# Optimization experiments

Hardware: AMD Instinct MI355X
Metric: run time of the kernel (lower is better)

Reference implementation:

```python
import jax, jax.numpy as jnp
import numpy as np

D_MODEL = 1024
N_HEADS = 16
HEAD_DIM = D_MODEL // N_HEADS


def setup_inputs() -> dict:
    key = jax.random.key(0)
    ks = jax.random.split(key, 5)
    x = jax.random.normal(ks[0], (2, 2048, D_MODEL), dtype=jnp.float32)
    s = 1.0 / np.sqrt(D_MODEL)
    W_qkv = jax.random.normal(ks[1], (D_MODEL, 3 * D_MODEL), dtype=jnp.float32) * s
    b_qkv = jnp.zeros((3 * D_MODEL,), dtype=jnp.float32)
    W_proj = jax.random.normal(ks[2], (D_MODEL, D_MODEL), dtype=jnp.float32) * s
    b_proj = jnp.zeros((D_MODEL,), dtype=jnp.float32)
    return {"x": x, "W_qkv": W_qkv, "b_qkv": b_qkv, "W_proj": W_proj, "b_proj": b_proj}


def reference(x, W_qkv, b_qkv, W_proj, b_proj):
    b, t, c = x.shape
    qkv = x @ W_qkv + b_qkv  # [b,t,3c]
    q, k, v = jnp.split(qkv, 3, axis=-1)
    # [b, h, t, d]
    q = q.reshape(b, t, N_HEADS, HEAD_DIM).transpose(0, 2, 1, 3)
    k = k.reshape(b, t, N_HEADS, HEAD_DIM).transpose(0, 2, 1, 3)
    v = v.reshape(b, t, N_HEADS, HEAD_DIM).transpose(0, 2, 1, 3)
    att = jnp.einsum('bhqd,bhkd->bhqk', q, k) / np.sqrt(HEAD_DIM)
    causal = jnp.tril(jnp.ones((t, t), dtype=bool))  # [t,t]
    att = jnp.where(causal[None, None], att, -jnp.inf)
    att = jax.nn.softmax(att, axis=-1)
    out = jnp.einsum('bhqk,bhkd->bhqd', att, v)  # [b,h,t,d]
    out = out.transpose(0, 2, 1, 3).reshape(b, t, c)
    return out @ W_proj + b_proj
```

## Files before the change

kernel.cpp:

```cpp
#include <hip/hip_runtime.h>
#include <hip/hip_bf16.h>

#define NB 2
#define NH 16
#define HD 64
#define DM 1024
#define TT 2048

typedef __attribute__((ext_vector_type(4))) float f32x4;
typedef __attribute__((ext_vector_type(8))) short bf16x8;

__device__ __forceinline__ unsigned short f2bf(float f) {
  union { float f; unsigned int i; } x; x.f = f;
  unsigned int r = x.i + 0x7fffu + ((x.i >> 16) & 1u);
  return (unsigned short)(r >> 16);
}

__device__ __forceinline__ unsigned int cvtpk(float lo, float hi) {
  unsigned int r;
  asm("v_cvt_pk_bf16_f32 %0, %1, %2" : "=v"(r) : "v"(lo), "v"(hi));
  return r;
}

__device__ __forceinline__ void async16(unsigned short* lds_base, const unsigned short* g) {
  __builtin_amdgcn_global_load_lds(
      (const __attribute__((address_space(1))) void*)g,
      (__attribute__((address_space(3))) void*)lds_base, 16, 0, 0);
}

__global__ __launch_bounds__(256)
void prep_kernel(const float* __restrict__ x, unsigned short* __restrict__ xbf,
                 const float* __restrict__ Wqkv, unsigned short* __restrict__ WqkvT,
                 const float* __restrict__ Wproj, unsigned short* __restrict__ WprojT)
{
  __shared__ unsigned short T[64][72];
  const int bid = blockIdx.x;
  const int t = threadIdx.x;

  if (bid < 2048) {
    const int i = bid * 256 + t;
    const f32x4 a = *(const f32x4*)(x + (size_t)i * 8);
    const f32x4 b = *(const f32x4*)(x + (size_t)i * 8 + 4);
    uint4 o;
    o.x = f2bf(a.x) | ((unsigned)f2bf(a.y) << 16);
    o.y = f2bf(a.z) | ((unsigned)f2bf(a.w) << 16);
    o.z = f2bf(b.x) | ((unsigned)f2bf(b.y) << 16);
    o.w = f2bf(b.z) | ((unsigned)f2bf(b.w) << 16);
    *(uint4*)(xbf + (size_t)i * 8) = o;
    return;
  }

  const float* W;
  unsigned short* WT;
  int n0, k0, N;
  if (bid < 2048 + 768) {
    const int li = bid - 2048;
    W = Wqkv; WT = WqkvT; N = 3 * DM;
    n0 = (li % 48) * 64; k0 = (li / 48) * 64;
  } else {
    const int li = bid - 2816;
    W = Wproj; WT = WprojT; N = DM;
    n0 = (li % 16) * 64; k0 = (li / 16) * 64;
  }
  const int r = t >> 2;
  const int c = (t & 3) * 16;
  const float* src = W + (size_t)(k0 + r) * N + n0 + c;
  #pragma unroll
  for (int s = 0; s < 4; ++s) {
    const f32x4 v = *(const f32x4*)(src + s * 4);
    T[c + s*4 + 0][r] = f2bf(v.x);
    T[c + s*4 + 1][r] = f2bf(v.y);
    T[c + s*4 + 2][r] = f2bf(v.z);
    T[c + s*4 + 3][r] = f2bf(v.w);
  }
  __syncthreads();
  unsigned short* dst = WT + (size_t)(n0 + r) * DM + k0 + c;
  *(uint4*)(dst)     = *(const uint4*)(&T[r][c]);
  *(uint4*)(dst + 8) = *(const uint4*)(&T[r][c + 8]);
}

__global__ __launch_bounds__(256)
void gemm_qkv(const unsigned short* __restrict__ A, const unsigned short* __restrict__ BT,
              const float* __restrict__ bias, unsigned short* __restrict__ Cout,
              int M, int N, int K)
{
  __shared__ unsigned short As[128 * 32];
  __shared__ unsigned short Bs[128 * 32];
  const int tid = threadIdx.x;
  const int lane = tid & 63;
  const int w = tid >> 6;
  const int wr = w >> 1, wc = w & 1;
  const int l15 = lane & 15, g = lane >> 4;

  const int gx = gridDim.x;
  const int li = blockIdx.y * gx + blockIdx.x;
  const int chunk = (gx * gridDim.y) >> 3;
  const int tile = (li & 7) * chunk + (li >> 3);
  const int m0 = (tile / gx) * 128;
  const int n0 = (tile % gx) * 128;

  f32x4 acc[4][4] = {};

  const int ar0 = tid >> 2,          as0 = (tid & 3) * 8;
  const int ar1 = (256 + tid) >> 2;
  const unsigned short* A0 = A + (size_t)(m0 + ar0) * K + as0;
  const unsigned short* A1 = A + (size_t)(m0 + ar1) * K + as0;
  const unsigned short* B0 = BT + (size_t)(n0 + ar0) * K + as0;
  const unsigned short* B1 = BT + (size_t)(n0 + ar1) * K + as0;
  unsigned short* AsW0 = &As[(0 * 256 + w * 64) * 8];
  unsigned short* AsW1 = &As[(1 * 256 + w * 64) * 8];
  unsigned short* BsW0 = &Bs[(0 * 256 + w * 64) * 8];
  unsigned short* BsW1 = &Bs[(1 * 256 + w * 64) * 8];

  for (int k0 = 0; k0 < K; k0 += 32) {
    async16(AsW0, A0 + k0);
    async16(AsW1, A1 + k0);
    async16(BsW0, B0 + k0);
    async16(BsW1, B1 + k0);
    __syncthreads();

    bf16x8 af[4], bfv[4];
    #pragma unroll
    for (int i = 0; i < 4; ++i)
      af[i] = *(const bf16x8*)(&As[(wr * 64 + i * 16 + l15) * 32 + g * 8]);
    #pragma unroll
    for (int j = 0; j < 4; ++j)
      bfv[j] = *(const bf16x8*)(&Bs[(wc * 64 + j * 16 + l15) * 32 + g * 8]);
    #pragma unroll
    for (int i = 0; i < 4; ++i)
      #pragma unroll
      for (int j = 0; j < 4; ++j)
        acc[i][j] = __builtin_amdgcn_mfma_f32_16x16x32_bf16(af[i], bfv[j], acc[i][j], 0, 0, 0);
    __syncthreads();
  }

  #pragma unroll
  for (int i = 0; i < 4; ++i) {
    #pragma unroll
    for (int j = 0; j < 4; ++j) {
      #pragma unroll
      for (int e = 0; e < 4; ++e) {
        const int row = m0 + wr * 64 + i * 16 + g * 4 + e;
        const int col = n0 + wc * 64 + j * 16 + l15;
        float val = acc[i][j][e] + bias[col];
        const int which = col >> 10;
        if (which == 0) val *= 0.125f;
        const int rem = col & 1023;
        const int hh = rem >> 6, dd = rem & 63;
        const int bb = row >> 11, tt = row & 2047;
        Cout[((((size_t)which * NB + bb) * NH + hh) * TT + tt) * HD + dd] = f2bf(val);
      }
    }
  }
}

__global__ __launch_bounds__(256)
void gemm_proj(const unsigned short* __restrict__ A, const unsigned short* __restrict__ BT,
               const float* __restrict__ bias, float* __restrict__ Cout,
               int M, int N, int K)
{
  __shared__ unsigned short As[128 * 32];
  __shared__ unsigned short Bs[64 * 32];
  const int tid = threadIdx.x;
  const int lane = tid & 63;
  const int w = tid >> 6;
  const int wr = w >> 1, wc = w & 1;
  const int l15 = lane & 15, g = lane >> 4;

  const int gx = gridDim.x;
  const int li = blockIdx.y * gx + blockIdx.x;
  const int chunk = (gx * gridDim.y) >> 3;
  const int tile = (li & 7) * chunk + (li >> 3);
  const int m0 = (tile / gx) * 128;
  const int n0 = (tile % gx) * 64;

  f32x4 acc[4][2] = {};

  const int ar0 = tid >> 2,          as0 = (tid & 3) * 8;
  const int ar1 = (256 + tid) >> 2;
  const unsigned short* A0 = A + (size_t)(m0 + ar0) * K + as0;
  const unsigned short* A1 = A + (size_t)(m0 + ar1) * K + as0;
  const unsigned short* B0 = BT + (size_t)(n0 + ar0) * K + as0;
  unsigned short* AsW0 = &As[(0 * 256 + w * 64) * 8];
  unsigned short* AsW1 = &As[(1 * 256 + w * 64) * 8];
  unsigned short* BsW0 = &Bs[(w * 64) * 8];

  for (int k0 = 0; k0 < K; k0 += 32) {
    async16(AsW0, A0 + k0);
    async16(AsW1, A1 + k0);
    async16(BsW0, B0 + k0);
    __syncthreads();

    bf16x8 af[4], bfv[2];
    #pragma unroll
    for (int i = 0; i < 4; ++i)
      af[i] = *(const bf16x8*)(&As[(wr * 64 + i * 16 + l15) * 32 + g * 8]);
    #pragma unroll
    for (int j = 0; j < 2; ++j)
      bfv[j] = *(const bf16x8*)(&Bs[(wc * 32 + j * 16 + l15) * 32 + g * 8]);
    #pragma unroll
    for (int i = 0; i < 4; ++i)
      #pragma unroll
      for (int j = 0; j < 2; ++j)
        acc[i][j] = __builtin_amdgcn_mfma_f32_16x16x32_bf16(af[i], bfv[j], acc[i][j], 0, 0, 0);
    __syncthreads();
  }

  #pragma unroll
  for (int i = 0; i < 4; ++i) {
    #pragma unroll
    for (int j = 0; j < 2; ++j) {
      #pragma unroll
      for (int e = 0; e < 4; ++e) {
        const int row = m0 + wr * 64 + i * 16 + g * 4 + e;
        const int col = n0 + wc * 32 + j * 16 + l15;
        Cout[(size_t)row * N + col] = acc[i][j][e] + bias[col];
      }
    }
  }
}

__global__ __launch_bounds__(512)
void attn_kernel(const unsigned short* __restrict__ qkv, unsigned short* __restrict__ attn_out)
{
  __shared__ unsigned short Ksm[64 * 72];
  __shared__ unsigned short VTsm[64 * 70];
  __shared__ unsigned short Psm[8][16 * 72];

  const int tid = threadIdx.x;
  const int lane = tid & 63;
  const int wv = tid >> 6;
  const int l15 = lane & 15;
  const int g = lane >> 4;

  const int li = blockIdx.x;
  const int xcd = li & 7;
  const int r = li >> 3;
  const int halfid = r >> 5;
  const int j = r & 31;
  const int bh = ((j >> 3) << 3) | xcd;
  const int jj = j & 7;
  const int qt = halfid ? (7 - jj) : (8 + jj);
  const int q0 = qt * 128;

  const size_t base = (size_t)bh * TT * HD;
  const unsigned short* Qg = qkv + base;
  const unsigned short* Kg = qkv + (size_t)NB * NH * TT * HD + base;
  const unsigned short* Vg = qkv + (size_t)2 * NB * NH * TT * HD + base;

  const int qw = q0 + wv * 16;
  const bf16x8 qf0 = *(const bf16x8*)(Qg + (size_t)(qw + l15) * HD + g * 8);
  const bf16x8 qf1 = *(const bf16x8*)(Qg + (size_t)(qw + l15) * HD + 32 + g * 8);

  f32x4 o[4] = {};
  float lsum = 0.f;

  const bool kRole = (wv < 4);
  const int krow = (tid & 255) >> 2;
  const int kseg = (tid & 3) * 16;
  const int vt   = tid & 255;
  const int vr0  = (vt >> 4) * 4;
  const int vc0  = (vt & 15) * 4;

  const int nt = 2 * qt + 2;

  uint4 st0, st1;
  {
    if (kRole) {
      const unsigned short* kp = Kg + (size_t)krow * HD + kseg;
      st0 = *(const uint4*)(kp);
      st1 = *(const uint4*)(kp + 8);
    } else {
      const uint2 a = *(const uint2*)(Vg + (size_t)(vr0 + 0) * HD + vc0);
      const uint2 b = *(const uint2*)(Vg + (size_t)(vr0 + 1) * HD + vc0);
      const uint2 c = *(const uint2*)(Vg + (size_t)(vr0 + 2) * HD + vc0);
      const uint2 d = *(const uint2*)(Vg + (size_t)(vr0 + 3) * HD + vc0);
      st0.x = a.x; st0.y = a.y; st0.z = b.x; st0.w = b.y;
      st1.x = c.x; st1.y = c.y; st1.z = d.x; st1.w = d.y;
    }
  }

  for (int t = 0; t < nt; ++t) {
    const int t0 = t * 64;
    __syncthreads();
    if (kRole) {
      *(uint4*)(&Ksm[krow * 72 + kseg])     = st0;
      *(uint4*)(&Ksm[krow * 72 + kseg + 8]) = st1;
    } else {
      unsigned short r0[4] = {(unsigned short)(st0.x & 0xffffu), (unsigned short)(st0.x >> 16),
                              (unsigned short)(st0.y & 0xffffu), (unsigned short)(st0.y >> 16)};
      unsigned short r1[4] = {(unsigned short)(st0.z & 0xffffu), (unsigned short)(st0.z >> 16),
                              (unsigned short)(st0.w & 0xffffu), (unsigned short)(st0.w >> 16)};
      unsigned short r2[4] = {(unsigned short)(st1.x & 0xffffu), (unsigned short)(st1.x >> 16),
                              (unsigned short)(st1.y & 0xffffu), (unsigned short)(st1.y >> 16)};
      unsigned short r3[4] = {(unsigned short)(st1.z & 0xffffu), (unsigned short)(st1.z >> 16),
                              (unsigned short)(st1.w & 0xffffu), (unsigned short)(st1.w >> 16)};
      #pragma unroll
      for (int c2 = 0; c2 < 4; ++c2) {
        ushort4 col;
        col.x = r0[c2]; col.y = r1[c2]; col.z = r2[c2]; col.w = r3[c2];
        *(ushort4*)(&VTsm[(vc0 + c2) * 70 + vr0]) = col;
      }
    }
    __syncthreads();

    if (t + 1 < nt) {
      const int t1 = t0 + 64;
      if (kRole) {
        const unsigned short* kp = Kg + (size_t)(t1 + krow) * HD + kseg;
        st0 = *(const uint4*)(kp);
        st1 = *(const uint4*)(kp + 8);
      } else {
        const uint2 a = *(const uint2*)(Vg + (size_t)(t1 + vr0 + 0) * HD + vc0);
        const uint2 b = *(const uint2*)(Vg + (size_t)(t1 + vr0 + 1) * HD + vc0);
        const uint2 c = *(const uint2*)(Vg + (size_t)(t1 + vr0 + 2) * HD + vc0);
        const uint2 d = *(const uint2*)(Vg + (size_t)(t1 + vr0 + 3) * HD + vc0);
        st0.x = a.x; st0.y = a.y; st0.z = b.x; st0.w = b.y;
        st1.x = c.x; st1.y = c.y; st1.z = d.x; st1.w = d.y;
      }
    }

    if (t0 <= qw + 15) {
      f32x4 sT[4] = {};
      __builtin_amdgcn_s_setprio(1);
      #pragma unroll
      for (int b = 0; b < 4; ++b) {
        const bf16x8 kf0 = *(const bf16x8*)(&Ksm[(b * 16 + l15) * 72 + g * 8]);
        const bf16x8 kf1 = *(const bf16x8*)(&Ksm[(b * 16 + l15) * 72 + 32 + g * 8]);
        sT[b] = __builtin_amdgcn_mfma_f32_16x16x32_bf16(kf0, qf0, sT[b], 0, 0, 0);
        sT[b] = __builtin_amdgcn_mfma_f32_16x16x32_bf16(kf1, qf1, sT[b], 0, 0, 0);
      }
      __builtin_amdgcn_s_setprio(0);

      if (t0 + 63 > qw) {
        #pragma unroll
        for (int b = 0; b < 4; ++b)
          #pragma unroll
          for (int e = 0; e < 4; ++e)
            if (t0 + b * 16 + 4 * g + e > qw + l15) sT[b][e] = -INFINITY;
      }

      #pragma unroll
      for (int b = 0; b < 4; ++b) {
        const float p0 = __expf(sT[b][0]);
        const float p1 = __expf(sT[b][1]);
        const float p2 = __expf(sT[b][2]);
        const float p3 = __expf(sT[b][3]);
        lsum += (p0 + p1) + (p2 + p3);
        uint2 wd; wd.x = cvtpk(p0, p1); wd.y = cvtpk(p2, p3);
        *(uint2*)(&Psm[wv][l15 * 72 + b * 16 + 4 * g]) = wd;
      }

      __builtin_amdgcn_s_setprio(1);
      #pragma unroll
      for (int c = 0; c < 2; ++c) {
        const bf16x8 pf = *(const bf16x8*)(&Psm[wv][l15 * 72 + c * 32 + g * 8]);
        #pragma unroll
        for (int db = 0; db < 4; ++db) {
          const bf16x8 vf = *(const bf16x8*)(&VTsm[(db * 16 + l15) * 70 + c * 32 + g * 8]);
          o[db] = __builtin_amdgcn_mfma_f32_16x16x32_bf16(pf, vf, o[db], 0, 0, 0);
        }
      }
      __builtin_amdgcn_s_setprio(0);
    }
  }

  lsum += __shfl_xor(lsum, 16, 64);
  lsum += __shfl_xor(lsum, 32, 64);

  const int bb = bh >> 4;
  const int hh = bh & 15;
  #pragma unroll
  for (int e = 0; e < 4; ++e) {
    const float inv = 1.f / __shfl(lsum, 4 * g + e, 64);
    const int q = qw + 4 * g + e;
    #pragma unroll
    for (int db = 0; db < 4; ++db)
      attn_out[(size_t)(bb * TT + q) * DM + hh * HD + db * 16 + l15] = f2bf(o[db][e] * inv);
  }
}

extern "C" void kernel_launch(void* const* d_in, const int* in_sizes, int n_in,
                              void* d_out, int out_size, void* d_ws, size_t ws_size,
                              hipStream_t stream)
{
  const float* x     = (const float*)d_in[0];
  const float* Wqkv  = (const float*)d_in[1];
  const float* bqkv  = (const float*)d_in[2];
  const float* Wproj = (const float*)d_in[3];
  const float* bproj = (const float*)d_in[4];

  const size_t qkv_elems = (size_t)3 * NB * NH * TT * HD;
  unsigned short* qkv_ws  = (unsigned short*)d_ws;
  unsigned short* WqkvT   = qkv_ws + qkv_elems;
  unsigned short* WprojT  = WqkvT + (size_t)3 * DM * DM;
  unsigned short* xbf     = WprojT + (size_t)DM * DM;
  unsigned short* attn_ws = xbf;

  hipLaunchKernelGGL(prep_kernel, dim3(3072, 1, 1), dim3(256), 0, stream,
                     x, xbf, Wqkv, WqkvT, Wproj, WprojT);
  hipLaunchKernelGGL(gemm_qkv, dim3(3 * DM / 128, NB * TT / 128, 1), dim3(256), 0, stream,
                     xbf, WqkvT, bqkv, qkv_ws, NB * TT, 3 * DM, DM);
  hipLaunchKernelGGL(attn_kernel, dim3(512, 1, 1), dim3(512), 0, stream,
                     qkv_ws, attn_ws);
  hipLaunchKernelGGL(gemm_proj, dim3(DM / 64, NB * TT / 128, 1), dim3(256), 0, stream,
                     attn_ws, WprojT, bproj, (float*)d_out, NB * TT, DM, DM);
}
```

Measured before the change: 119.4 us.

## Double-buffer K/V LDS tiles in attention to halve barriers per tile

Splits the K and transposed-V shared-memory tiles into two buffers and unrolls the key-tile loop by two. The next tile is written to the alternate buffer while the current one is being computed, so each tile needs one __syncthreads instead of two. This targets barrier stalls and lets global-load latency overlap with MFMA work. In exchange it uses more LDS per block, which could reduce occupancy, and it assumes the tile count is even (nt = 2*qt+2 always is).

```diff
diff --git a/kernel.cpp b/kernel.cpp
--- a/kernel.cpp
+++ b/kernel.cpp
@@ -223,8 +223,10 @@
 __global__ __launch_bounds__(512)
 void attn_kernel(const unsigned short* __restrict__ qkv, unsigned short* __restrict__ attn_out)
 {
-  __shared__ unsigned short Ksm[64 * 72];
-  __shared__ unsigned short VTsm[64 * 70];
+  __shared__ unsigned short Ksm0[64 * 72];
+  __shared__ unsigned short Ksm1[64 * 72];
+  __shared__ unsigned short VT0[64 * 70];
+  __shared__ unsigned short VT1[64 * 70];
   __shared__ unsigned short Psm[8][16 * 72];
 
   const int tid = threadIdx.x;
@@ -265,27 +267,26 @@
   const int nt = 2 * qt + 2;
 
   uint4 st0, st1;
-  {
+
+  auto load_regs = [&](const int tb) {
     if (kRole) {
-      const unsigned short* kp = Kg + (size_t)krow * HD + kseg;
+      const unsigned short* kp = Kg + (size_t)(tb + krow) * HD + kseg;
       st0 = *(const uint4*)(kp);
       st1 = *(const uint4*)(kp + 8);
     } else {
-      const uint2 a = *(const uint2*)(Vg + (size_t)(vr0 + 0) * HD + vc0);
-      const uint2 b = *(const uint2*)(Vg + (size_t)(vr0 + 1) * HD + vc0);
-      const uint2 c = *(const uint2*)(Vg + (size_t)(vr0 + 2) * HD + vc0);
-      const uint2 d = *(const uint2*)(Vg + (size_t)(vr0 + 3) * HD + vc0);
+      const uint2 a = *(const uint2*)(Vg + (size_t)(tb + vr0 + 0) * HD + vc0);
+      const uint2 b = *(const uint2*)(Vg + (size_t)(tb + vr0 + 1) * HD + vc0);
+      const uint2 c = *(const uint2*)(Vg + (size_t)(tb + vr0 + 2) * HD + vc0);
+      const uint2 d = *(const uint2*)(Vg + (size_t)(tb + vr0 + 3) * HD + vc0);
       st0.x = a.x; st0.y = a.y; st0.z = b.x; st0.w = b.y;
       st1.x = c.x; st1.y = c.y; st1.z = d.x; st1.w = d.y;
     }
-  }
-
-  for (int t = 0; t < nt; ++t) {
-    const int t0 = t * 64;
-    __syncthreads();
+  };
+
+  auto write_lds = [&](unsigned short* kbuf, unsigned short* vbuf) {
     if (kRole) {
-      *(uint4*)(&Ksm[krow * 72 + kseg])     = st0;
-      *(uint4*)(&Ksm[krow * 72 + kseg + 8]) = st1;
+      *(uint4*)(&kbuf[krow * 72 + kseg])     = st0;
+      *(uint4*)(&kbuf[krow * 72 + kseg + 8]) = st1;
     } else {
       unsigned short r0[4] = {(unsigned short)(st0.x & 0xffffu), (unsigned short)(st0.x >> 16),
                               (unsigned short)(st0.y & 0xffffu), (unsigned short)(st0.y >> 16)};
@@ -299,70 +300,72 @@
       for (int c2 = 0; c2 < 4; ++c2) {
         ushort4 col;
         col.x = r0[c2]; col.y = r1[c2]; col.z = r2[c2]; col.w = r3[c2];
-        *(ushort4*)(&VTsm[(vc0 + c2) * 70 + vr0]) = col;
+        *(ushort4*)(&vbuf[(vc0 + c2) * 70 + vr0]) = col;
       }
     }
-    __syncthreads();
-
-    if (t + 1 < nt) {
-      const int t1 = t0 + 64;
-      if (kRole) {
-        const unsigned short* kp = Kg + (size_t)(t1 + krow) * HD + kseg;
-        st0 = *(const uint4*)(kp);
-        st1 = *(const uint4*)(kp + 8);
-      } else {
-        const uint2 a = *(const uint2*)(Vg + (size_t)(t1 + vr0 + 0) * HD + vc0);
-        const uint2 b = *(const uint2*)(Vg + (size_t)(t1 + vr0 + 1) * HD + vc0);
-        const uint2 c = *(const uint2*)(Vg + (size_t)(t1 + vr0 + 2) * HD + vc0);
-        const uint2 d = *(const uint2*)(Vg + (size_t)(t1 + vr0 + 3) * HD + vc0);
-        st0.x = a.x; st0.y = a.y; st0.z = b.x; st0.w = b.y;
-        st1.x = c.x; st1.y = c.y; st1.z = d.x; st1.w = d.y;
+  };
+
+  auto compute_tile = [&](const int t0, const unsigned short* kb, const unsigned short* vb) {
+    if (t0 > qw + 15) return;
+    f32x4 sT[4] = {};
+    __builtin_amdgcn_s_setprio(1);
+    #pragma unroll
+    for (int b = 0; b < 4; ++b) {
+      const bf16x8 kf0 = *(const bf16x8*)(&kb[(b * 16 + l15) * 72 + g * 8]);
+      const bf16x8 kf1 = *(const bf16x8*)(&kb[(b * 16 + l15) * 72 + 32 + g * 8]);
+      sT[b] = __builtin_amdgcn_mfma_f32_16x16x32_bf16(kf0, qf0, sT[b], 0, 0, 0);
+      sT[b] = __builtin_amdgcn_mfma_f32_16x16x32_bf16(kf1, qf1, sT[b], 0, 0, 0);
+    }
+    __builtin_amdgcn_s_setprio(0);
+
+    if (t0 + 63 > qw) {
+      #pragma unroll
+      for (int b = 0; b < 4; ++b)
+        #pragma unroll
+        for (int e = 0; e < 4; ++e)
+          if (t0 + b * 16 + 4 * g + e > qw + l15) sT[b][e] = -INFINITY;
+    }
+
+    #pragma unroll
+    for (int b = 0; b < 4; ++b) {
+      const float p0 = __expf(sT[b][0]);
+      const float p1 = __expf(sT[b][1]);
+      const float p2 = __expf(sT[b][2]);
+      const float p3 = __expf(sT[b][3]);
+      lsum += (p0 + p1) + (p2 + p3);
+      uint2 wd; wd.x = cvtpk(p0, p1); wd.y = cvtpk(p2, p3);
+      *(uint2*)(&Psm[wv][l15 * 72 + b * 16 + 4 * g]) = wd;
+    }
+
+    __builtin_amdgcn_s_setprio(1);
+    #pragma unroll
+    for (int c = 0; c < 2; ++c) {
+      const bf16x8 pf = *(const bf16x8*)(&Psm[wv][l15 * 72 + c * 32 + g * 8]);
+      #pragma unroll
+      for (int db = 0; db < 4; ++db) {
+        const bf16x8 vf = *(const bf16x8*)(&vb[(db * 16 + l15) * 70 + c * 32 + g * 8]);
+        o[db] = __builtin_amdgcn_mfma_f32_16x16x32_bf16(pf, vf, o[db], 0, 0, 0);
       }
     }
-
-    if (t0 <= qw + 15) {
-      f32x4 sT[4] = {};
-      __builtin_amdgcn_s_setprio(1);
-      #pragma unroll
-      for (int b = 0; b < 4; ++b) {
-        const bf16x8 kf0 = *(const bf16x8*)(&Ksm[(b * 16 + l15) * 72 + g * 8]);
-        const bf16x8 kf1 = *(const bf16x8*)(&Ksm[(b * 16 + l15) * 72 + 32 + g * 8]);
-        sT[b] = __builtin_amdgcn_mfma_f32_16x16x32_bf16(kf0, qf0, sT[b], 0, 0, 0);
-        sT[b] = __builtin_amdgcn_mfma_f32_16x16x32_bf16(kf1, qf1, sT[b], 0, 0, 0);
-      }
-      __builtin_amdgcn_s_setprio(0);
-
-      if (t0 + 63 > qw) {
-        #pragma unroll
-        for (int b = 0; b < 4; ++b)
-          #pragma unroll
-          for (int e = 0; e < 4; ++e)
-            if (t0 + b * 16 + 4 * g + e > qw + l15) sT[b][e] = -INFINITY;
-      }
-
-      #pragma unroll
-      for (int b = 0; b < 4; ++b) {
-        const float p0 = __expf(sT[b][0]);
-        const float p1 = __expf(sT[b][1]);
-        const float p2 = __expf(sT[b][2]);
-        const float p3 = __expf(sT[b][3]);
-        lsum += (p0 + p1) + (p2 + p3);
-        uint2 wd; wd.x = cvtpk(p0, p1); wd.y = cvtpk(p2, p3);
-        *(uint2*)(&Psm[wv][l15 * 72 + b * 16 + 4 * g]) = wd;
-      }
-
-      __builtin_amdgcn_s_setprio(1);
-      #pragma unroll
-      for (int c = 0; c < 2; ++c) {
-        const bf16x8 pf = *(const bf16x8*)(&Psm[wv][l15 * 72 + c * 32 + g * 8]);
-        #pragma unroll
-        for (int db = 0; db < 4; ++db) {
-          const bf16x8 vf = *(const bf16x8*)(&VTsm[(db * 16 + l15) * 70 + c * 32 + g * 8]);
-          o[db] = __builtin_amdgcn_mfma_f32_16x16x32_bf16(pf, vf, o[db], 0, 0, 0);
-        }
-      }
-      __builtin_amdgcn_s_setprio(0);
-    }
+    __builtin_amdgcn_s_setprio(0);
+  };
+
+  load_regs(0);
+  write_lds(Ksm0, VT0);
+  __syncthreads();
+
+  const int np = nt >> 1;
+  for (int tp = 0; tp < np; ++tp) {
+    const int t = 2 * tp;
+    load_regs((t + 1) * 64);
+    compute_tile(t * 64, Ksm0, VT0);
+    write_lds(Ksm1, VT1);
+    __syncthreads();
+    const bool more = (t + 2 < nt);
+    if (more) load_regs((t + 2) * 64);
+    compute_tile((t + 1) * 64, Ksm1, VT1);
+    if (more) write_lds(Ksm0, VT0);
+    __syncthreads();
   }
 
   lsum += __shfl_xor(lsum, 16, 64);
```

Measured after the change: 163.6 us. +37.0%, slower.
